# Kernel optimization log

Hardware: AMD Instinct MI355X
Metric: run time of the kernel (lower is better)

## Reference

```python
import jax, jax.numpy as jnp
import numpy as np

EMBED = 1024
HEADS = 16
HDIM = EMBED // HEADS
WIN = 14
RANK = 16
ALPHA = 32
MLP = 4 * EMBED


def setup_inputs() -> dict:
    key = jax.random.key(0)
    ks = jax.random.split(key, 10)
    s = 0.02
    return {
        "x": jax.random.normal(ks[0], (2, 64, 64, EMBED), jnp.float32),
        "norm1_g": jnp.ones((EMBED,), jnp.float32),
        "norm1_b": jnp.zeros((EMBED,), jnp.float32),
        "qkv_w": jax.random.normal(ks[1], (EMBED, 3 * EMBED), jnp.float32) * s,
        "qkv_b": jnp.zeros((3 * EMBED,), jnp.float32),
        "lora_a": jax.random.normal(ks[2], (EMBED, RANK), jnp.float32) * s,
        "lora_b": jax.random.normal(ks[3], (RANK, 3 * EMBED), jnp.float32) * s,
        "rel_pos_h": jax.random.normal(ks[4], (2 * WIN - 1, HDIM), jnp.float32) * s,
        "rel_pos_w": jax.random.normal(ks[5], (2 * WIN - 1, HDIM), jnp.float32) * s,
        "proj_w": jax.random.normal(ks[6], (EMBED, EMBED), jnp.float32) * s,
        "proj_b": jnp.zeros((EMBED,), jnp.float32),
        "norm2_g": jnp.ones((EMBED,), jnp.float32),
        "norm2_b": jnp.zeros((EMBED,), jnp.float32),
        "mlp_w1": jax.random.normal(ks[7], (EMBED, MLP), jnp.float32) * s,
        "mlp_b1": jnp.zeros((MLP,), jnp.float32),
        "mlp_w2": jax.random.normal(ks[8], (MLP, EMBED), jnp.float32) * s,
        "mlp_b2": jnp.zeros((EMBED,), jnp.float32),
    }


def layer_norm(x, g, b, eps=1e-6):
    mu = jnp.mean(x, axis=-1, keepdims=True)
    var = jnp.var(x, axis=-1, keepdims=True)
    return (x - mu) * jax.lax.rsqrt(var + eps) * g + b


def window_partition(x, w):
    B, H, W, C = x.shape
    ph, pw = (w - H % w) % w, (w - W % w) % w
    x = jnp.pad(x, ((0, 0), (0, ph), (0, pw), (0, 0)))
    Hp, Wp = H + ph, W + pw
    x = x.reshape(B, Hp // w, w, Wp // w, w, C)
    x = x.transpose(0, 1, 3, 2, 4, 5).reshape(-1, w, w, C)
    return x, (Hp, Wp)


def window_unpartition(x, w, pad_hw, hw):
    Hp, Wp = pad_hw
    H, W = hw
    B = x.shape[0] // (Hp // w * (Wp // w))
    x = x.reshape(B, Hp // w, Wp // w, w, w, -1)
    x = x.transpose(0, 1, 3, 2, 4, 5).reshape(B, Hp, Wp, -1)
    return x[:, :H, :W, :]


def _rel_table(rel_pos, size):
    # square windows, no interpolation: table is (2*size-1, dim)
    idx = jnp.arange(size)[:, None] - jnp.arange(size)[None, :] + (size - 1)
    return rel_pos[idx]  # (size, size, dim)


def reference(x, norm1_g, norm1_b, qkv_w, qkv_b, lora_a, lora_b,
              rel_pos_h, rel_pos_w, proj_w, proj_b, norm2_g, norm2_b,
              mlp_w1, mlp_b1, mlp_w2, mlp_b2):
    shortcut = x
    xn = layer_norm(x, norm1_g, norm1_b)
    h, w = xn.shape[1], xn.shape[2]
    xw, pad_hw = window_partition(xn, WIN)
    Bw, H, W, C = xw.shape
    N = H * W
    xf = xw.reshape(Bw, N, C)
    # QKV with LoRA injection: qkv(x) + (x @ A @ B) * alpha/rank
    qkv = xf @ qkv_w + qkv_b + (xf @ lora_a @ lora_b) * (ALPHA / RANK)
    qkv = qkv.reshape(Bw, N, 3, HEADS, HDIM).transpose(2, 0, 3, 1, 4)  # 3,Bw,h,N,d
    q, k, v = qkv[0], qkv[1], qkv[2]
    scale = HDIM ** -0.5
    attn = jnp.einsum('bhnd,bhmd->bhnm', q * scale, k)  # (Bw,heads,N,N)
    # decomposed relative position bias
    Rh = _rel_table(rel_pos_h, H)  # (H,H,d)
    Rw = _rel_table(rel_pos_w, W)  # (W,W,d)
    rq = q.reshape(Bw, HEADS, H, W, HDIM)
    rel_h = jnp.einsum('bhxyd,xkd->bhxyk', rq, Rh)  # (Bw,heads,H,W,H)
    rel_w = jnp.einsum('bhxyd,ykd->bhxyk', rq, Rw)  # (Bw,heads,H,W,W)
    attn = (attn.reshape(Bw, HEADS, H, W, H, W)
            + rel_h[..., :, None] + rel_w[..., None, :]).reshape(Bw, HEADS, N, N)
    attn = jax.nn.softmax(attn, axis=-1)
    out = jnp.einsum('bhnm,bhmd->bhnd', attn, v)
    out = out.reshape(Bw, HEADS, H, W, HDIM).transpose(0, 2, 3, 1, 4).reshape(Bw, H, W, C)
    out = out @ proj_w + proj_b
    out = window_unpartition(out, WIN, pad_hw, (h, w))
    x = shortcut + out
    # MLP with exact GELU (torch default)
    xn2 = layer_norm(x, norm2_g, norm2_b)
    hmid = jax.nn.gelu(xn2 @ mlp_w1 + mlp_b1, approximate=False)
    x = x + (hmid @ mlp_w2 + mlp_b2)
    return x
```

## Files before the change

kernel.cpp:

```cpp
#include <hip/hip_runtime.h>
#include <cstdint>
#include <cstddef>


typedef __bf16 bf16x8 __attribute__((ext_vector_type(8)));
typedef float f32x4 __attribute__((ext_vector_type(4)));

__device__ __forceinline__ unsigned short f2bf(float f) {
    unsigned u = __float_as_uint(f);
    u = (u + 0x7fffu + ((u >> 16) & 1u)) >> 16;
    return (unsigned short)u;
}
__device__ __forceinline__ float bf2f(unsigned short h) {
    return __uint_as_float(((unsigned)h) << 16);
}

#define GLDS16(gp, lp) __builtin_amdgcn_global_load_lds( \
    (__attribute__((address_space(1))) unsigned int*)(gp), \
    (__attribute__((address_space(3))) unsigned int*)(lp), 16, 0, 0)

__global__ __launch_bounds__(256) void weff_kernel(
    const float* __restrict__ W, const float* __restrict__ la,
    const float* __restrict__ lb, unsigned short* __restrict__ Wt)
{
    __shared__ float tile[32][33];
    __shared__ float lat[32][16];
    __shared__ float lbt[16][32];
    const int kb = blockIdx.x * 32, nb = blockIdx.y * 32;
    const int tn = threadIdx.x & 31, tk = threadIdx.x >> 5;
    for (int i = threadIdx.x; i < 32 * 16; i += 256)
        lat[i >> 4][i & 15] = la[(size_t)(kb + (i >> 4)) * 16 + (i & 15)];
    for (int i = threadIdx.x; i < 16 * 32; i += 256)
        lbt[i >> 5][i & 31] = lb[(size_t)(i >> 5) * 3072 + nb + (i & 31)];
#pragma unroll
    for (int i = 0; i < 4; ++i) {
        int k = tk + i * 8;
        tile[k][tn] = W[(size_t)(kb + k) * 3072 + nb + tn];
    }
    __syncthreads();
#pragma unroll
    for (int i = 0; i < 4; ++i) {
        int n = tk + i * 8;
        float acc = tile[tn][n];
#pragma unroll
        for (int r = 0; r < 16; ++r) acc += 2.0f * lat[tn][r] * lbt[r][n];
        Wt[(size_t)(nb + n) * 1024 + kb + tn] = f2bf(acc);
    }
}

__global__ __launch_bounds__(256) void transpose_bf16_kernel(
    const float* __restrict__ W, unsigned short* __restrict__ Wt,
    int Kdim, int Ndim)
{
    __shared__ float tile[32][33];
    const int kb = blockIdx.x * 32, nb = blockIdx.y * 32;
    const int tn = threadIdx.x & 31, tk = threadIdx.x >> 5;
#pragma unroll
    for (int i = 0; i < 4; ++i) {
        int k = tk + i * 8;
        tile[k][tn] = W[(size_t)(kb + k) * Ndim + nb + tn];
    }
    __syncthreads();
#pragma unroll
    for (int i = 0; i < 4; ++i) {
        int n = tk + i * 8;
        Wt[(size_t)(nb + n) * Kdim + kb + tn] = f2bf(tile[tn][n]);
    }
}

__global__ __launch_bounds__(256) void ln1_kernel(
    const float* __restrict__ x, const float* __restrict__ g,
    const float* __restrict__ b, unsigned short* __restrict__ out)
{
    const int blk = blockIdx.x;
    const int tid = threadIdx.x;
    const int bw = blk / 196, tok = blk - bw * 196;
    const int bat = bw / 25, rw = bw - bat * 25;
    const int wy = rw / 5, wx = rw - wy * 5;
    const int ty = tok / 14, tx = tok - ty * 14;
    const int y = wy * 14 + ty, xx = wx * 14 + tx;
    unsigned short* orow = out + (size_t)blk * 1024;
    if (y >= 64 || xx >= 64) {
        *(uint2*)(orow + tid * 4) = make_uint2(0u, 0u);
        return;
    }
    const float* irow = x + ((size_t)((bat * 64 + y) * 64 + xx)) * 1024;
    const float4 v = *(const float4*)(irow + tid * 4);
    float s = v.x + v.y + v.z + v.w;
    float ss = v.x * v.x + v.y * v.y + v.z * v.z + v.w * v.w;
    for (int o = 32; o > 0; o >>= 1) { s += __shfl_xor(s, o); ss += __shfl_xor(ss, o); }
    __shared__ float red[8];
    const int wave = tid >> 6, lane = tid & 63;
    if (lane == 0) { red[wave] = s; red[4 + wave] = ss; }
    __syncthreads();
    s = red[0] + red[1] + red[2] + red[3];
    ss = red[4] + red[5] + red[6] + red[7];
    const float mu = s * (1.0f / 1024.0f);
    const float var = ss * (1.0f / 1024.0f) - mu * mu;
    const float rstd = rsqrtf(var + 1e-6f);
    const float4 gv = *(const float4*)(g + tid * 4);
    const float4 bv = *(const float4*)(b + tid * 4);
    const float a0 = (v.x - mu) * rstd * gv.x + bv.x;
    const float a1 = (v.y - mu) * rstd * gv.y + bv.y;
    const float a2 = (v.z - mu) * rstd * gv.z + bv.z;
    const float a3 = (v.w - mu) * rstd * gv.w + bv.w;
    const unsigned r0 = (unsigned)f2bf(a0) | ((unsigned)f2bf(a1) << 16);
    const unsigned r1 = (unsigned)f2bf(a2) | ((unsigned)f2bf(a3) << 16);
    *(uint2*)(orow + tid * 4) = make_uint2(r0, r1);
}

__global__ __launch_bounds__(256) void ln2_kernel(
    const float* __restrict__ x, const float* __restrict__ g,
    const float* __restrict__ b, unsigned short* __restrict__ out)
{
    const int blk = blockIdx.x;
    const int tid = threadIdx.x;
    const float* irow = x + (size_t)blk * 1024;
    unsigned short* orow = out + (size_t)blk * 1024;
    const float4 v = *(const float4*)(irow + tid * 4);
    float s = v.x + v.y + v.z + v.w;
    float ss = v.x * v.x + v.y * v.y + v.z * v.z + v.w * v.w;
    for (int o = 32; o > 0; o >>= 1) { s += __shfl_xor(s, o); ss += __shfl_xor(ss, o); }
    __shared__ float red[8];
    const int wave = tid >> 6, lane = tid & 63;
    if (lane == 0) { red[wave] = s; red[4 + wave] = ss; }
    __syncthreads();
    s = red[0] + red[1] + red[2] + red[3];
    ss = red[4] + red[5] + red[6] + red[7];
    const float mu = s * (1.0f / 1024.0f);
    const float var = ss * (1.0f / 1024.0f) - mu * mu;
    const float rstd = rsqrtf(var + 1e-6f);
    const float4 gv = *(const float4*)(g + tid * 4);
    const float4 bv = *(const float4*)(b + tid * 4);
    const float a0 = (v.x - mu) * rstd * gv.x + bv.x;
    const float a1 = (v.y - mu) * rstd * gv.y + bv.y;
    const float a2 = (v.z - mu) * rstd * gv.z + bv.z;
    const float a3 = (v.w - mu) * rstd * gv.w + bv.w;
    const unsigned r0 = (unsigned)f2bf(a0) | ((unsigned)f2bf(a1) << 16);
    const unsigned r1 = (unsigned)f2bf(a2) | ((unsigned)f2bf(a3) << 16);
    *(uint2*)(orow + tid * 4) = make_uint2(r0, r1);
}

template <int EPI, int KS>
__global__ __launch_bounds__(512, 2) void gemm8p_v2(
    const unsigned short* __restrict__ A,
    const unsigned short* __restrict__ Bt,
    const float* __restrict__ bias,
    void* __restrict__ outp,
    const float* __restrict__ aux,
    int M, int K, int nbm, int nbn)
{
    constexpr int ABUF = 256 * 64;
    constexpr int BBUF = 256 * 64;

    __shared__ unsigned short As_s[2 * ABUF];
    __shared__ unsigned short Bs_s[2 * BBUF];

    const int tid = threadIdx.x;
    const int wave = tid >> 6, lane = tid & 63;
    const int lr = lane & 15, lq = lane >> 4;

    const int ss = (nbm + 7) >> 3;
    const int xcd = blockIdx.x & 7;
    const int sidx = blockIdx.x >> 3;
    const int ntl2 = sidx / ss;
    const int m_loc = sidx - ntl2 * ss;
    const int mt = xcd * ss + m_loc;
    if (mt >= nbm) return;
    int ks = 0, ntl = ntl2;
    if constexpr (KS > 1) {
        ks = ntl2 / nbn;
        ntl = ntl2 - ks * nbn;
    }
    const int m_base = mt * 256, n_base = ntl * 256;
    const int Kp = K / KS;
    const int kb = ks * Kp;
    const int NT = Kp >> 6;

    const int wm = (wave >> 2) * 128;
    const int wn = (wave & 3) * 64;

    const unsigned short* a_src[4];
    const unsigned short* b_src[4];
#pragma unroll
    for (int i = 0; i < 4; ++i) {
        const int p = i * 512 + tid;
        const int row = p >> 3, sl = p & 7;
        const int g = (((sl >> 2) ^ (row & 1)) << 2) | ((sl & 3) ^ ((row >> 1) & 3));
        int gr = m_base + row; gr = gr < M ? gr : M - 1;
        a_src[i] = A + (size_t)gr * K + kb + g * 8;
        b_src[i] = Bt + (size_t)(n_base + row) * K + kb + g * 8;
    }

#define STAGE_ALL(kt) do { \
        unsigned short* _ad = As_s + (((kt) & 1) ? ABUF : 0) + tid * 8; \
        unsigned short* _bd = Bs_s + (((kt) & 1) ? BBUF : 0) + tid * 8; \
        GLDS16(a_src[0] + (size_t)(kt) * 64, _ad); \
        GLDS16(b_src[0] + (size_t)(kt) * 64, _bd); \
        GLDS16(a_src[1] + (size_t)(kt) * 64, _ad + 4096); \
        GLDS16(b_src[1] + (size_t)(kt) * 64, _bd + 4096); \
        GLDS16(a_src[2] + (size_t)(kt) * 64, _ad + 8192); \
        GLDS16(b_src[2] + (size_t)(kt) * 64, _bd + 8192); \
        GLDS16(a_src[3] + (size_t)(kt) * 64, _ad + 12288); \
        GLDS16(b_src[3] + (size_t)(kt) * 64, _bd + 12288); \
    } while (0)

    const int frsw = ((lr & 1) << 2) | (lq ^ ((lr >> 1) & 3));
    const int a_off = (wm + lr) * 64 + frsw * 8;
    const int b_off = (wn + lr) * 64 + frsw * 8;

    f32x4 acc[8][4] = {};

    STAGE_ALL(0);
    asm volatile("s_waitcnt vmcnt(0)" ::: "memory");
    __builtin_amdgcn_s_barrier();

    for (int t = 0; t < NT; ++t) {
        const unsigned short* Ab = As_s + (t & 1) * ABUF;
        const unsigned short* Bb = Bs_s + (t & 1) * BBUF;
        bf16x8 afr[4], bfr[4];
#pragma unroll
        for (int mf = 0; mf < 4; ++mf) afr[mf] = *(const bf16x8*)(Ab + a_off + mf * 1024);
#pragma unroll
        for (int nf = 0; nf < 4; ++nf) bfr[nf] = *(const bf16x8*)(Bb + b_off + nf * 1024);
        if (t + 1 < NT) STAGE_ALL(t + 1);
        __builtin_amdgcn_s_barrier();
        asm volatile("s_waitcnt lgkmcnt(0)" ::: "memory");
        __builtin_amdgcn_s_setprio(1);
#pragma unroll
        for (int mf = 0; mf < 4; ++mf)
#pragma unroll
            for (int nf = 0; nf < 4; ++nf)
                acc[mf][nf] = __builtin_amdgcn_mfma_f32_16x16x32_bf16(afr[mf], bfr[nf], acc[mf][nf], 0, 0, 0);
        __builtin_amdgcn_s_setprio(0);
        __builtin_amdgcn_s_barrier();
#pragma unroll
        for (int mf = 0; mf < 4; ++mf) afr[mf] = *(const bf16x8*)(Ab + a_off + (4 + mf) * 1024);
        __builtin_amdgcn_s_barrier();
        asm volatile("s_waitcnt lgkmcnt(0)" ::: "memory");
        __builtin_amdgcn_s_setprio(1);
#pragma unroll
        for (int mf = 0; mf < 4; ++mf)
#pragma unroll
            for (int nf = 0; nf < 4; ++nf)
                acc[4 + mf][nf] = __builtin_amdgcn_mfma_f32_16x16x32_bf16(afr[mf], bfr[nf], acc[4 + mf][nf], 0, 0, 0);
        __builtin_amdgcn_s_setprio(0);
        __builtin_amdgcn_s_barrier();
#pragma unroll
        for (int mf = 0; mf < 4; ++mf) afr[mf] = *(const bf16x8*)(Ab + (a_off ^ 32) + mf * 1024);
#pragma unroll
        for (int nf = 0; nf < 4; ++nf) bfr[nf] = *(const bf16x8*)(Bb + (b_off ^ 32) + nf * 1024);
        __builtin_amdgcn_s_barrier();
        asm volatile("s_waitcnt lgkmcnt(0)" ::: "memory");
        __builtin_amdgcn_s_setprio(1);
#pragma unroll
        for (int mf = 0; mf < 4; ++mf)
#pragma unroll
            for (int nf = 0; nf < 4; ++nf)
                acc[mf][nf] = __builtin_amdgcn_mfma_f32_16x16x32_bf16(afr[mf], bfr[nf], acc[mf][nf], 0, 0, 0);
        __builtin_amdgcn_s_setprio(0);
        __builtin_amdgcn_s_barrier();
#pragma unroll
        for (int mf = 0; mf < 4; ++mf) afr[mf] = *(const bf16x8*)(Ab + (a_off ^ 32) + (4 + mf) * 1024);
        __builtin_amdgcn_s_barrier();
        asm volatile("s_waitcnt lgkmcnt(0)" ::: "memory");
        __builtin_amdgcn_s_setprio(1);
#pragma unroll
        for (int mf = 0; mf < 4; ++mf)
#pragma unroll
            for (int nf = 0; nf < 4; ++nf)
                acc[4 + mf][nf] = __builtin_amdgcn_mfma_f32_16x16x32_bf16(afr[mf], bfr[nf], acc[4 + mf][nf], 0, 0, 0);
        __builtin_amdgcn_s_setprio(0);
        asm volatile("s_waitcnt vmcnt(0)" ::: "memory");
        __builtin_amdgcn_s_barrier();
    }
#undef STAGE_ALL

    float biasv[4];
#pragma unroll
    for (int j = 0; j < 4; ++j)
        biasv[j] = (KS == 1 || ks == 0) ? bias[n_base + wn + j * 16 + lr] : 0.0f;

    if constexpr (EPI == 0) {
#pragma unroll
        for (int i = 0; i < 8; ++i) {
            const int m0i = m_base + wm + i * 16 + lq * 4;
            if (m0i >= M) continue;
            const int bw = m0i / 196, tok0 = m0i - bw * 196;
#pragma unroll
            for (int j = 0; j < 4; ++j) {
                const int n = n_base + wn + j * 16 + lr;
                const int which = n >> 10, hh = (n >> 6) & 15, d = n & 63;
                unsigned short* slotp = (unsigned short*)outp + (size_t)((bw * 3 + which) * 16 + hh) * 13312;
                if (which == 2) {
                    unsigned long long pv = 0;
#pragma unroll
                    for (int r = 0; r < 4; ++r)
                        pv |= (unsigned long long)f2bf(acc[i][j][r] + biasv[j]) << (16 * r);
                    *(unsigned long long*)(slotp + (size_t)d * 208 + tok0) = pv;
                } else {
#pragma unroll
                    for (int r = 0; r < 4; ++r)
                        slotp[(size_t)(tok0 + r) * 64 + d] = f2bf(acc[i][j][r] + biasv[j]);
                }
            }
        }
    } else {
#pragma unroll
        for (int i = 0; i < 8; ++i) {
#pragma unroll
            for (int r = 0; r < 4; ++r) {
                const int m = m_base + wm + i * 16 + lq * 4 + r;
                if (m >= M) continue;
#pragma unroll
                for (int j = 0; j < 4; ++j) {
                    const int n = n_base + wn + j * 16 + lr;
                    const float v = acc[i][j][r] + biasv[j];
                    if constexpr (EPI == 2) {
                        const float t2 = 1.5957691216f * (v + 0.044715f * v * v * v);
                        const float e = __expf(-t2);
                        const float gl = v * __builtin_amdgcn_rcpf(1.0f + e);
                        ((unsigned short*)outp)[(size_t)m * 4096 + n] = f2bf(gl);
                    } else {
                        atomicAdd(&((float*)outp)[(size_t)m * 1024 + n], v);
                    }
                }
            }
        }
    }
    (void)aux;
}

template <int EPI>
__global__ __launch_bounds__(256) void gemm_kernel(
    const unsigned short* __restrict__ A,
    const unsigned short* __restrict__ Bt,
    const float* __restrict__ bias,
    void* __restrict__ outp,
    const float* __restrict__ aux,
    int M, int K, int nbm, int nbn)
{
    __shared__ unsigned short As[2][128 * 32];
    __shared__ unsigned short Bs[2][128 * 32];
    const int tid = threadIdx.x;
    const int wave = tid >> 6, lane = tid & 63;
    const int lr = lane & 15, lq = lane >> 4;
    const int ss = (nbm + 7) >> 3;
    const int xcd = blockIdx.x & 7;
    const int s = blockIdx.x >> 3;
    const int nt = s / ss;
    const int m_loc = s - nt * ss;
    const int mt = xcd * ss + m_loc;
    if (mt >= nbm) return;
    const int m_base = mt * 128, n_base = nt * 128;
    const int wm = (wave >> 1) * 64, wn = (wave & 1) * 64;
    const int N = nbn * 128;

    const int c0 = tid, c1 = tid + 256;
    const int row0 = c0 >> 2, row1 = c1 >> 2;
    const int kc = (tid & 3) ^ ((tid >> 3) & 3);
    int ar0 = m_base + row0; ar0 = ar0 < M ? ar0 : M - 1;
    int ar1 = m_base + row1; ar1 = ar1 < M ? ar1 : M - 1;
    int br0 = n_base + row0; br0 = br0 < N ? br0 : N - 1;
    int br1 = n_base + row1; br1 = br1 < N ? br1 : N - 1;
    const unsigned short* agp0 = A + (size_t)ar0 * K + kc * 8;
    const unsigned short* agp1 = A + (size_t)ar1 * K + kc * 8;
    const unsigned short* bgp0 = Bt + (size_t)br0 * K + kc * 8;
    const unsigned short* bgp1 = Bt + (size_t)br1 * K + kc * 8;
    unsigned short* alp0 = As[0] + c0 * 8;
    unsigned short* alp1 = As[0] + c1 * 8;
    unsigned short* blp0 = Bs[0] + c0 * 8;
    unsigned short* blp1 = Bs[0] + c1 * 8;
    unsigned short* alp0b = As[1] + c0 * 8;
    unsigned short* alp1b = As[1] + c1 * 8;
    unsigned short* blp0b = Bs[1] + c0 * 8;
    unsigned short* blp1b = Bs[1] + c1 * 8;

    const int swz = (lq ^ ((lr >> 1) & 3)) * 8;

    f32x4 acc[4][4] = {};

    for (int k0 = 0; k0 < K; k0 += 64) {
        GLDS16(agp0 + k0, alp0);
        GLDS16(agp1 + k0, alp1);
        GLDS16(bgp0 + k0, blp0);
        GLDS16(bgp1 + k0, blp1);
        GLDS16(agp0 + k0 + 32, alp0b);
        GLDS16(agp1 + k0 + 32, alp1b);
        GLDS16(bgp0 + k0 + 32, blp0b);
        GLDS16(bgp1 + k0 + 32, blp1b);
        __syncthreads();
#pragma unroll
        for (int half = 0; half < 2; ++half) {
            bf16x8 af[4], bfr[4];
#pragma unroll
            for (int i = 0; i < 4; ++i) {
                af[i]  = *(const bf16x8*)(As[half] + (wm + i * 16 + lr) * 32 + swz);
                bfr[i] = *(const bf16x8*)(Bs[half] + (wn + i * 16 + lr) * 32 + swz);
            }
#pragma unroll
            for (int i = 0; i < 4; ++i)
#pragma unroll
                for (int j = 0; j < 4; ++j)
                    acc[i][j] = __builtin_amdgcn_mfma_f32_16x16x32_bf16(af[i], bfr[j], acc[i][j], 0, 0, 0);
        }
        __syncthreads();
    }

    float biasv[4];
#pragma unroll
    for (int j = 0; j < 4; ++j) biasv[j] = bias[n_base + wn + j * 16 + lr];

#pragma unroll
    for (int i = 0; i < 4; ++i) {
#pragma unroll
        for (int r = 0; r < 4; ++r) {
            const int m = m_base + wm + i * 16 + lq * 4 + r;
            if (m >= M) continue;
            int y = 0, xx = 0, b = 0;
            if constexpr (EPI == 1) {
                const int bw = m / 196, tok = m - bw * 196;
                b = bw / 25;
                const int rw = bw - b * 25;
                const int wy = rw / 5, wx = rw - wy * 5;
                const int ty = tok / 14, tx = tok - ty * 14;
                y = wy * 14 + ty; xx = wx * 14 + tx;
            }
#pragma unroll
            for (int j = 0; j < 4; ++j) {
                const int n = n_base + wn + j * 16 + lr;
                const float v = acc[i][j][r] + biasv[j];
                if constexpr (EPI == 1) {
                    if (y < 64 && xx < 64) {
                        const size_t idx = ((size_t)((b * 64 + y) * 64 + xx)) * 1024 + n;
                        ((float*)outp)[idx] = aux[idx] + v;
                    }
                } else {
                    const size_t idx = (size_t)m * 1024 + n;
                    ((float*)outp)[idx] += v;
                }
            }
        }
    }
}

__global__ __launch_bounds__(256, 2) void attn_kernel(
    const unsigned short* __restrict__ qkv,
    const float* __restrict__ relh, const float* __restrict__ relw,
    unsigned short* __restrict__ attn_out)
{
    __shared__ unsigned short Vt[64][232];
    __shared__ unsigned short Pst[4][16][232];
    __shared__ unsigned short Db[196][28];

    const int tid = threadIdx.x;
    const int wave = tid >> 6, lane = tid & 63;
    const int lr = lane & 15, lq = lane >> 4;
    const int bw = blockIdx.x >> 4, h = blockIdx.x & 15;
    const unsigned short* qp = qkv + (size_t)((bw * 3 + 0) * 16 + h) * 13312;
    const unsigned short* kp = qkv + (size_t)((bw * 3 + 1) * 16 + h) * 13312;
    const unsigned short* vp = qkv + (size_t)((bw * 3 + 2) * 16 + h) * 13312;

    *(uint2*)&Pst[wave][lane >> 2][208 + (lane & 3) * 4] = make_uint2(0u, 0u);

    {
        unsigned short* vtf = &Vt[0][0];
        for (int idx = tid; idx < 64 * 29; idx += 256) {
            const int d = idx / 29, c = idx - d * 29;
            GLDS16(vp + d * 208 + c * 8, vtf + idx * 8);
        }
    }

    for (int t = wave; t < 28; t += 4) {
        const int isw = t >= 14;
        const int c = isw ? t - 14 : t;
        const int arow = isw ? (lr * 14 + c) : (c * 14 + lr);
        const unsigned short* ap = qp + arow * 64 + lq * 8;
        const bf16x8 a0 = *(const bf16x8*)ap;
        const bf16x8 a1 = *(const bf16x8*)(ap + 32);
        int ridx = c - lr + 13;
        ridx = ridx < 0 ? 0 : (ridx > 26 ? 26 : ridx);
        const float* tb = (isw ? relw : relh) + ridx * 64 + lq * 8;
        union BV { unsigned short u[8]; bf16x8 v; } b0, b1;
        {
            const float4 x0 = *(const float4*)tb;
            const float4 x1 = *(const float4*)(tb + 4);
            b0.u[0] = f2bf(x0.x); b0.u[1] = f2bf(x0.y); b0.u[2] = f2bf(x0.z); b0.u[3] = f2bf(x0.w);
            b0.u[4] = f2bf(x1.x); b0.u[5] = f2bf(x1.y); b0.u[6] = f2bf(x1.z); b0.u[7] = f2bf(x1.w);
            const float4 x2 = *(const float4*)(tb + 32);
            const float4 x3 = *(const float4*)(tb + 36);
            b1.u[0] = f2bf(x2.x); b1.u[1] = f2bf(x2.y); b1.u[2] = f2bf(x2.z); b1.u[3] = f2bf(x2.w);
            b1.u[4] = f2bf(x3.x); b1.u[5] = f2bf(x3.y); b1.u[6] = f2bf(x3.z); b1.u[7] = f2bf(x3.w);
        }
        f32x4 dacc = {};
        dacc = __builtin_amdgcn_mfma_f32_16x16x32_bf16(a0, b0.v, dacc, 0, 0, 0);
        dacc = __builtin_amdgcn_mfma_f32_16x16x32_bf16(a1, b1.v, dacc, 0, 0, 0);
#pragma unroll
        for (int r = 0; r < 4; ++r) {
            const int y = lq * 4 + r;
            if (y < 14 && lr < 14) {
                const int g = isw ? y * 14 + c : c * 14 + y;
                Db[g][isw ? 14 + lr : lr] = f2bf(dacc[r]);
            }
        }
    }
    __syncthreads();

    for (int mt = wave; mt < 13; mt += 4) {
        const int m0 = mt * 16;
        const unsigned short* qb = qp + (size_t)(m0 + lr) * 64 + lq * 8;
        const bf16x8 qa0 = *(const bf16x8*)qb;
        const bf16x8 qa1 = *(const bf16x8*)(qb + 32);
        f32x4 sc[13];
#pragma unroll
        for (int nt = 0; nt < 13; ++nt) {
            const unsigned short* kb = kp + (size_t)(nt * 16 + lr) * 64 + lq * 8;
            const bf16x8 k0 = *(const bf16x8*)kb;
            const bf16x8 k1 = *(const bf16x8*)(kb + 32);
            f32x4 a = {};
            a = __builtin_amdgcn_mfma_f32_16x16x32_bf16(qa0, k0, a, 0, 0, 0);
            a = __builtin_amdgcn_mfma_f32_16x16x32_bf16(qa1, k1, a, 0, 0, 0);
            sc[nt] = a;
        }
        int grow[4];
#pragma unroll
        for (int r = 0; r < 4; ++r) {
            int g = m0 + lq * 4 + r;
            grow[r] = g > 195 ? 195 : g;
        }
#pragma unroll
        for (int nt = 0; nt < 13; ++nt) {
            const int n = nt * 16 + lr;
            if (n < 196) {
                const int nx = n / 14, ny = n - nx * 14;
#pragma unroll
                for (int r = 0; r < 4; ++r)
                    sc[nt][r] = sc[nt][r] * 0.125f + bf2f(Db[grow[r]][nx]) + bf2f(Db[grow[r]][14 + ny]);
            } else {
#pragma unroll
                for (int r = 0; r < 4; ++r) sc[nt][r] = -1e30f;
            }
        }
        float rs[4];
#pragma unroll
        for (int r = 0; r < 4; ++r) {
            float mx = sc[0][r];
#pragma unroll
            for (int nt = 1; nt < 13; ++nt) mx = fmaxf(mx, sc[nt][r]);
            mx = fmaxf(mx, __shfl_xor(mx, 1));
            mx = fmaxf(mx, __shfl_xor(mx, 2));
            mx = fmaxf(mx, __shfl_xor(mx, 4));
            mx = fmaxf(mx, __shfl_xor(mx, 8));
            float s = 0.f;
#pragma unroll
            for (int nt = 0; nt < 13; ++nt) {
                const float e = __expf(sc[nt][r] - mx);
                sc[nt][r] = e;
                s += e;
            }
            s += __shfl_xor(s, 1);
            s += __shfl_xor(s, 2);
            s += __shfl_xor(s, 4);
            s += __shfl_xor(s, 8);
            rs[r] = 1.0f / s;
        }
#pragma unroll
        for (int nt = 0; nt < 13; ++nt)
#pragma unroll
            for (int r = 0; r < 4; ++r)
                Pst[wave][lq * 4 + r][nt * 16 + lr] = f2bf(sc[nt][r]);
#pragma unroll
        for (int dt = 0; dt < 4; ++dt) {
            f32x4 a = {};
#pragma unroll
            for (int ks = 0; ks < 7; ++ks) {
                const bf16x8 pa = *(const bf16x8*)&Pst[wave][lr][ks * 32 + lq * 8];
                const bf16x8 vb = *(const bf16x8*)&Vt[dt * 16 + lr][ks * 32 + lq * 8];
                a = __builtin_amdgcn_mfma_f32_16x16x32_bf16(pa, vb, a, 0, 0, 0);
            }
#pragma unroll
            for (int r = 0; r < 4; ++r) {
                const int m = m0 + lq * 4 + r;
                if (m < 196)
                    attn_out[(size_t)(bw * 196 + m) * 1024 + h * 64 + dt * 16 + lr] = f2bf(a[r] * rs[r]);
            }
        }
    }
}

extern "C" void kernel_launch(void* const* d_in, const int* in_sizes, int n_in,
                              void* d_out, int out_size, void* d_ws, size_t ws_size,
                              hipStream_t stream)
{
    (void)in_sizes; (void)n_in; (void)out_size; (void)ws_size;
    const float* x      = (const float*)d_in[0];
    const float* n1g    = (const float*)d_in[1];
    const float* n1b    = (const float*)d_in[2];
    const float* qkv_w  = (const float*)d_in[3];
    const float* qkv_b  = (const float*)d_in[4];
    const float* lora_a = (const float*)d_in[5];
    const float* lora_b = (const float*)d_in[6];
    const float* relh   = (const float*)d_in[7];
    const float* relw   = (const float*)d_in[8];
    const float* proj_w = (const float*)d_in[9];
    const float* proj_b = (const float*)d_in[10];
    const float* n2g    = (const float*)d_in[11];
    const float* n2b    = (const float*)d_in[12];
    const float* w1     = (const float*)d_in[13];
    const float* b1     = (const float*)d_in[14];
    const float* w2     = (const float*)d_in[15];
    const float* b2     = (const float*)d_in[16];
    float* out = (float*)d_out;

    char* ws = (char*)d_ws;
    size_t off = 0;
    auto alloc = [&](size_t bytes) {
        char* p = ws + off;
        off += (bytes + 255) & ~(size_t)255;
        return p;
    };
    unsigned short* weffT = (unsigned short*)alloc((size_t)3072 * 1024 * 2);
    unsigned short* projT = (unsigned short*)alloc((size_t)1024 * 1024 * 2);
    unsigned short* w1T   = (unsigned short*)alloc((size_t)4096 * 1024 * 2);
    unsigned short* w2T   = (unsigned short*)alloc((size_t)1024 * 4096 * 2);
    unsigned short* xnw   = (unsigned short*)alloc((size_t)9800 * 1024 * 2);
    unsigned short* qkvb  = (unsigned short*)alloc((size_t)8192 * 4096 * 2);
    unsigned short* attno = (unsigned short*)alloc((size_t)9800 * 1024 * 2);

    weff_kernel<<<dim3(32, 96), 256, 0, stream>>>(qkv_w, lora_a, lora_b, weffT);
    transpose_bf16_kernel<<<dim3(32, 32), 256, 0, stream>>>(proj_w, projT, 1024, 1024);
    transpose_bf16_kernel<<<dim3(32, 128), 256, 0, stream>>>(w1, w1T, 1024, 4096);
    transpose_bf16_kernel<<<dim3(128, 32), 256, 0, stream>>>(w2, w2T, 4096, 1024);
    ln1_kernel<<<9800, 256, 0, stream>>>(x, n1g, n1b, xnw);
    gemm8p_v2<0, 1><<<dim3(8 * 5 * 12), 512, 0, stream>>>(xnw, weffT, qkv_b, qkvb, nullptr, 9800, 1024, 39, 12);
    attn_kernel<<<800, 256, 0, stream>>>(qkvb, relh, relw, attno);
    gemm_kernel<1><<<dim3(8 * 10 * 8), 256, 0, stream>>>(attno, projT, proj_b, out, x, 9800, 1024, 77, 8);
    unsigned short* xn2 = xnw;
    ln2_kernel<<<8192, 256, 0, stream>>>(out, n2g, n2b, xn2);
    unsigned short* hmid = qkvb;
    gemm8p_v2<2, 1><<<dim3(8 * 4 * 16), 512, 0, stream>>>(xn2, w1T, b1, hmid, nullptr, 8192, 1024, 32, 16);
    gemm8p_v2<3, 2><<<dim3(8 * 4 * 8), 512, 0, stream>>>(hmid, w2T, b2, out, nullptr, 8192, 4096, 32, 4);
}
```

Before: 597.1 us.

## Interleave next-tile global-to-LDS loads across MFMA phases in 256x256 GEMM

Rewrites the 8-wave bf16 GEMM main loop so the next K-tile's global_load_lds requests are split into four pairs, each issued in a different MFMA phase, instead of all being issued at the start. Partial vmcnt waits replace the full drain at the end of each iteration. The LDS swizzle changes to a simple 8-way XOR pattern, and the sub-tile compute order is reordered so the k-halves alternate per M-half. Sched barriers are added to keep the compiler from moving the LDS reads past the MFMA blocks. The risk is that the hand-counted vmcnt values are wrong, which would cause a race on the double buffer.

```diff
diff --git a/kernel.cpp b/kernel.cpp
--- a/kernel.cpp
+++ b/kernel.cpp
@@ -142,19 +142,15 @@
 }
 
 template <int EPI, int KS>
-__global__ __launch_bounds__(512, 2) void gemm8p_v2(
+__global__ __launch_bounds__(512, 2) void gemm8p_v3(
     const unsigned short* __restrict__ A,
     const unsigned short* __restrict__ Bt,
     const float* __restrict__ bias,
     void* __restrict__ outp,
-    const float* __restrict__ aux,
     int M, int K, int nbm, int nbn)
 {
-    constexpr int ABUF = 256 * 64;
-    constexpr int BBUF = 256 * 64;
-
-    __shared__ unsigned short As_s[2 * ABUF];
-    __shared__ unsigned short Bs_s[2 * BBUF];
+    __shared__ unsigned short As_s[2 * 16384];
+    __shared__ unsigned short Bs_s[2 * 16384];
 
     const int tid = threadIdx.x;
     const int wave = tid >> 6, lane = tid & 63;
@@ -168,113 +164,113 @@
     const int mt = xcd * ss + m_loc;
     if (mt >= nbm) return;
     int ks = 0, ntl = ntl2;
-    if constexpr (KS > 1) {
-        ks = ntl2 / nbn;
-        ntl = ntl2 - ks * nbn;
-    }
+    if constexpr (KS > 1) { ks = ntl2 / nbn; ntl = ntl2 - ks * nbn; }
     const int m_base = mt * 256, n_base = ntl * 256;
-    const int Kp = K / KS;
-    const int kb = ks * Kp;
+    const int Kp = K / KS, kb = ks * Kp;
     const int NT = Kp >> 6;
 
     const int wm = (wave >> 2) * 128;
     const int wn = (wave & 3) * 64;
 
-    const unsigned short* a_src[4];
-    const unsigned short* b_src[4];
-#pragma unroll
-    for (int i = 0; i < 4; ++i) {
-        const int p = i * 512 + tid;
-        const int row = p >> 3, sl = p & 7;
-        const int g = (((sl >> 2) ^ (row & 1)) << 2) | ((sl & 3) ^ ((row >> 1) & 3));
-        int gr = m_base + row; gr = gr < M ? gr : M - 1;
-        a_src[i] = A + (size_t)gr * K + kb + g * 8;
-        b_src[i] = Bt + (size_t)(n_base + row) * K + kb + g * 8;
-    }
-
-#define STAGE_ALL(kt) do { \
-        unsigned short* _ad = As_s + (((kt) & 1) ? ABUF : 0) + tid * 8; \
-        unsigned short* _bd = Bs_s + (((kt) & 1) ? BBUF : 0) + tid * 8; \
-        GLDS16(a_src[0] + (size_t)(kt) * 64, _ad); \
-        GLDS16(b_src[0] + (size_t)(kt) * 64, _bd); \
-        GLDS16(a_src[1] + (size_t)(kt) * 64, _ad + 4096); \
-        GLDS16(b_src[1] + (size_t)(kt) * 64, _bd + 4096); \
-        GLDS16(a_src[2] + (size_t)(kt) * 64, _ad + 8192); \
-        GLDS16(b_src[2] + (size_t)(kt) * 64, _bd + 8192); \
-        GLDS16(a_src[3] + (size_t)(kt) * 64, _ad + 12288); \
-        GLDS16(b_src[3] + (size_t)(kt) * 64, _bd + 12288); \
-    } while (0)
-
-    const int frsw = ((lr & 1) << 2) | (lq ^ ((lr >> 1) & 3));
-    const int a_off = (wm + lr) * 64 + frsw * 8;
-    const int b_off = (wn + lr) * 64 + frsw * 8;
+    const int srow = tid >> 3, sslot = tid & 7;
+    const int gch = sslot ^ (srow & 7);
+    const unsigned short* a_gp[4];
+    const unsigned short* b_gp[4];
+#pragma unroll
+    for (int u = 0; u < 4; ++u) {
+        int ar = m_base + u * 64 + srow; ar = ar < M ? ar : M - 1;
+        a_gp[u] = A + (size_t)ar * K + kb + gch * 8;
+        b_gp[u] = Bt + (size_t)(n_base + u * 64 + srow) * K + kb + gch * 8;
+    }
+#define STG_A(t, u) GLDS16(a_gp[u] + (size_t)(t) * 64, As_s + (((t) & 1) << 14) + (u) * 4096 + tid * 8)
+#define STG_B(t, u) GLDS16(b_gp[u] + (size_t)(t) * 64, Bs_s + (((t) & 1) << 14) + (u) * 4096 + tid * 8)
+
+    const int sl0 = lq ^ (lr & 7);
+    const int a_off = (wm + lr) * 64 + sl0 * 8;
+    const int b_off = (wn + lr) * 64 + sl0 * 8;
 
     f32x4 acc[8][4] = {};
 
-    STAGE_ALL(0);
-    asm volatile("s_waitcnt vmcnt(0)" ::: "memory");
+    STG_A(0, 0); STG_A(0, 2);
+    STG_B(0, 0); STG_B(0, 1); STG_B(0, 2); STG_B(0, 3);
+    STG_A(0, 1); STG_A(0, 3);
+    asm volatile("s_waitcnt vmcnt(2)" ::: "memory");
     __builtin_amdgcn_s_barrier();
 
     for (int t = 0; t < NT; ++t) {
-        const unsigned short* Ab = As_s + (t & 1) * ABUF;
-        const unsigned short* Bb = Bs_s + (t & 1) * BBUF;
-        bf16x8 afr[4], bfr[4];
-#pragma unroll
-        for (int mf = 0; mf < 4; ++mf) afr[mf] = *(const bf16x8*)(Ab + a_off + mf * 1024);
-#pragma unroll
-        for (int nf = 0; nf < 4; ++nf) bfr[nf] = *(const bf16x8*)(Bb + b_off + nf * 1024);
-        if (t + 1 < NT) STAGE_ALL(t + 1);
+        const unsigned short* Ab = As_s + ((t & 1) << 14);
+        const unsigned short* Bb = Bs_s + ((t & 1) << 14);
+        bf16x8 af[4], bfv[4];
+#pragma unroll
+        for (int mf = 0; mf < 4; ++mf) af[mf] = *(const bf16x8*)(Ab + a_off + mf * 1024);
+#pragma unroll
+        for (int nf = 0; nf < 4; ++nf) bfv[nf] = *(const bf16x8*)(Bb + b_off + nf * 1024);
+        if (t + 1 < NT) { STG_A(t + 1, 0); STG_A(t + 1, 2); }
         __builtin_amdgcn_s_barrier();
         asm volatile("s_waitcnt lgkmcnt(0)" ::: "memory");
+        __builtin_amdgcn_sched_barrier(0);
         __builtin_amdgcn_s_setprio(1);
 #pragma unroll
         for (int mf = 0; mf < 4; ++mf)
 #pragma unroll
             for (int nf = 0; nf < 4; ++nf)
-                acc[mf][nf] = __builtin_amdgcn_mfma_f32_16x16x32_bf16(afr[mf], bfr[nf], acc[mf][nf], 0, 0, 0);
+                acc[mf][nf] = __builtin_amdgcn_mfma_f32_16x16x32_bf16(af[mf], bfv[nf], acc[mf][nf], 0, 0, 0);
         __builtin_amdgcn_s_setprio(0);
         __builtin_amdgcn_s_barrier();
 #pragma unroll
-        for (int mf = 0; mf < 4; ++mf) afr[mf] = *(const bf16x8*)(Ab + a_off + (4 + mf) * 1024);
+        for (int mf = 0; mf < 4; ++mf) af[mf] = *(const bf16x8*)(Ab + (a_off ^ 32) + mf * 1024);
+#pragma unroll
+        for (int nf = 0; nf < 4; ++nf) bfv[nf] = *(const bf16x8*)(Bb + (b_off ^ 32) + nf * 1024);
+        if (t + 1 < NT) { STG_B(t + 1, 0); STG_B(t + 1, 1); }
         __builtin_amdgcn_s_barrier();
         asm volatile("s_waitcnt lgkmcnt(0)" ::: "memory");
+        __builtin_amdgcn_sched_barrier(0);
         __builtin_amdgcn_s_setprio(1);
 #pragma unroll
         for (int mf = 0; mf < 4; ++mf)
 #pragma unroll
             for (int nf = 0; nf < 4; ++nf)
-                acc[4 + mf][nf] = __builtin_amdgcn_mfma_f32_16x16x32_bf16(afr[mf], bfr[nf], acc[4 + mf][nf], 0, 0, 0);
+                acc[mf][nf] = __builtin_amdgcn_mfma_f32_16x16x32_bf16(af[mf], bfv[nf], acc[mf][nf], 0, 0, 0);
         __builtin_amdgcn_s_setprio(0);
-        __builtin_amdgcn_s_barrier();
-#pragma unroll
-        for (int mf = 0; mf < 4; ++mf) afr[mf] = *(const bf16x8*)(Ab + (a_off ^ 32) + mf * 1024);
-#pragma unroll
-        for (int nf = 0; nf < 4; ++nf) bfr[nf] = *(const bf16x8*)(Bb + (b_off ^ 32) + nf * 1024);
+        if (t == NT - 1) { asm volatile("s_waitcnt vmcnt(0)" ::: "memory"); }
+        else             { asm volatile("s_waitcnt vmcnt(4)" ::: "memory"); }
+        __builtin_amdgcn_s_barrier();
+#pragma unroll
+        for (int mf = 0; mf < 4; ++mf) af[mf] = *(const bf16x8*)(Ab + a_off + (4 + mf) * 1024);
+#pragma unroll
+        for (int nf = 0; nf < 4; ++nf) bfv[nf] = *(const bf16x8*)(Bb + b_off + nf * 1024);
+        if (t + 1 < NT) { STG_B(t + 1, 2); STG_B(t + 1, 3); }
         __builtin_amdgcn_s_barrier();
         asm volatile("s_waitcnt lgkmcnt(0)" ::: "memory");
+        __builtin_amdgcn_sched_barrier(0);
         __builtin_amdgcn_s_setprio(1);
 #pragma unroll
         for (int mf = 0; mf < 4; ++mf)
 #pragma unroll
             for (int nf = 0; nf < 4; ++nf)
-                acc[mf][nf] = __builtin_amdgcn_mfma_f32_16x16x32_bf16(afr[mf], bfr[nf], acc[mf][nf], 0, 0, 0);
+                acc[4 + mf][nf] = __builtin_amdgcn_mfma_f32_16x16x32_bf16(af[mf], bfv[nf], acc[4 + mf][nf], 0, 0, 0);
         __builtin_amdgcn_s_setprio(0);
         __builtin_amdgcn_s_barrier();
 #pragma unroll
-        for (int mf = 0; mf < 4; ++mf) afr[mf] = *(const bf16x8*)(Ab + (a_off ^ 32) + (4 + mf) * 1024);
+        for (int mf = 0; mf < 4; ++mf) af[mf] = *(const bf16x8*)(Ab + (a_off ^ 32) + (4 + mf) * 1024);
+#pragma unroll
+        for (int nf = 0; nf < 4; ++nf) bfv[nf] = *(const bf16x8*)(Bb + (b_off ^ 32) + nf * 1024);
+        if (t + 1 < NT) { STG_A(t + 1, 1); STG_A(t + 1, 3); }
         __builtin_amdgcn_s_barrier();
         asm volatile("s_waitcnt lgkmcnt(0)" ::: "memory");
+        __builtin_amdgcn_sched_barrier(0);
         __builtin_amdgcn_s_setprio(1);
 #pragma unroll
         for (int mf = 0; mf < 4; ++mf)
 #pragma unroll
             for (int nf = 0; nf < 4; ++nf)
-                acc[4 + mf][nf] = __builtin_amdgcn_mfma_f32_16x16x32_bf16(afr[mf], bfr[nf], acc[4 + mf][nf], 0, 0, 0);
+                acc[4 + mf][nf] = __builtin_amdgcn_mfma_f32_16x16x32_bf16(af[mf], bfv[nf], acc[4 + mf][nf], 0, 0, 0);
         __builtin_amdgcn_s_setprio(0);
-        asm volatile("s_waitcnt vmcnt(0)" ::: "memory");
-        __builtin_amdgcn_s_barrier();
-    }
-#undef STAGE_ALL
+        asm volatile("s_waitcnt vmcnt(2)" ::: "memory");
+        __builtin_amdgcn_s_barrier();
+    }
+#undef STG_A
+#undef STG_B
 
     float biasv[4];
 #pragma unroll
@@ -328,7 +324,6 @@
             }
         }
     }
-    (void)aux;
 }
 
 template <int EPI>
@@ -632,12 +627,12 @@
     transpose_bf16_kernel<<<dim3(32, 128), 256, 0, stream>>>(w1, w1T, 1024, 4096);
     transpose_bf16_kernel<<<dim3(128, 32), 256, 0, stream>>>(w2, w2T, 4096, 1024);
     ln1_kernel<<<9800, 256, 0, stream>>>(x, n1g, n1b, xnw);
-    gemm8p_v2<0, 1><<<dim3(8 * 5 * 12), 512, 0, stream>>>(xnw, weffT, qkv_b, qkvb, nullptr, 9800, 1024, 39, 12);
+    gemm8p_v3<0, 1><<<dim3(8 * 5 * 12), 512, 0, stream>>>(xnw, weffT, qkv_b, qkvb, 9800, 1024, 39, 12);
     attn_kernel<<<800, 256, 0, stream>>>(qkvb, relh, relw, attno);
     gemm_kernel<1><<<dim3(8 * 10 * 8), 256, 0, stream>>>(attno, projT, proj_b, out, x, 9800, 1024, 77, 8);
     unsigned short* xn2 = xnw;
     ln2_kernel<<<8192, 256, 0, stream>>>(out, n2g, n2b, xn2);
     unsigned short* hmid = qkvb;
-    gemm8p_v2<2, 1><<<dim3(8 * 4 * 16), 512, 0, stream>>>(xn2, w1T, b1, hmid, nullptr, 8192, 1024, 32, 16);
-    gemm8p_v2<3, 2><<<dim3(8 * 4 * 8), 512, 0, stream>>>(hmid, w2T, b2, out, nullptr, 8192, 4096, 32, 4);
-}
+    gemm8p_v3<2, 1><<<dim3(8 * 4 * 16), 512, 0, stream>>>(xn2, w1T, b1, hmid, 8192, 1024, 32, 16);
+    gemm8p_v3<3, 2><<<dim3(8 * 4 * 8), 512, 0, stream>>>(hmid, w2T, b2, out, 8192, 4096, 32, 4);
+}
```

After: 574.3 us. -3.8%, faster.
